# Performance work log

Measured on AMD Instinct MI355X. Metric: run time of the kernel, lower is better.

## Reference

```python
import jax, jax.numpy as jnp
import numpy as np

B, P, K, D, T = 512, 64, 8, 512, 50000


def setup_inputs() -> dict:
    key = jax.random.key(0)
    k1, k2, k3, k4, k5, k6 = jax.random.split(key, 6)
    return {
        "inputs": jax.random.normal(k1, (B, P, D), dtype=jnp.float32),
        "title_emb_mat": jax.random.normal(k2, (T, D), dtype=jnp.float32),
        "nbr_batch": jax.random.randint(k3, (B, P, K), 0, B, dtype=jnp.int32),
        "nbr_job": jax.random.randint(k4, (B, P, K), 0, P, dtype=jnp.int32),
        "nbr_title": jax.random.randint(k5, (B, P, K), 0, T, dtype=jnp.int32),
        "nbr_mask": jax.random.randint(k6, (B, P, K), 0, 2, dtype=jnp.int32),
    }


def reference(inputs, title_emb_mat, nbr_batch, nbr_job, nbr_title, nbr_mask):
    # inputs:        [B, P, D]  job embeddings per employee position
    # title_emb_mat: [T, Dt]    title embedding table (Dt == D here)
    # nbr_*:         [B, P, K]  padded metapath neighbor indices + validity mask
    mask = nbr_mask.astype(bool)                              # [B,P,K]
    ref_embs = inputs[nbr_batch, nbr_job]                     # [B,P,K,D] gather of neighbor job embs
    # attention logits: focal emb vs neighbor embs (raw inner product, exp-normalized)
    raw_s = jnp.einsum('bpd,bpkd->bpk', inputs, ref_embs)     # [B,P,K]
    logits = jnp.where(mask, raw_s, jnp.float32(-1e9))
    sim = jax.nn.softmax(logits, axis=-1) * mask              # exact zeros on padded slots;
    # an all-masked (i,pos) -> uniform softmax * 0 mask == 0 row (matches torch 'continue' -> zeros)
    ref_t_embs = title_emb_mat[nbr_title]                     # [B,P,K,Dt] gather of target-title embs
    graph_concat = jnp.einsum('bpk,bpkt->bpt', sim, ref_t_embs)  # [B,P,Dt]
    out = jnp.concatenate([inputs, graph_concat], axis=-1)    # [B,P,D+Dt]
    return out.reshape(B * P, D + title_emb_mat.shape[1])     # torch.cat over batch, axis=0
```

## Files before the change

kernel.cpp:

```cpp
#include <hip/hip_runtime.h>

#define BB 512
#define PP 64
#define KK 8
#define DD 512

typedef float v4f __attribute__((ext_vector_type(4)));


__device__ __forceinline__ void async_1k(const void* g, void* l) {
    __builtin_amdgcn_global_load_lds(
        (const __attribute__((address_space(1))) void*)g,
        (__attribute__((address_space(3))) void*)l,
        16, 0, 0);
}

__global__ __launch_bounds__(64) void han_meta_kernel(
    const float* __restrict__ inputs,
    const float* __restrict__ title,
    const int*   __restrict__ nbr_batch,
    const int*   __restrict__ nbr_job,
    const int*   __restrict__ nbr_title,
    const int*   __restrict__ nbr_mask,
    float*       __restrict__ out)
{
    __shared__ float lds_f[8192];

    const int lane = threadIdx.x;
    const int row  = __builtin_amdgcn_readfirstlane(blockIdx.x);

    const int* nb = nbr_batch + row * KK;
    const int* nj = nbr_job   + row * KK;
    const int* nt = nbr_title + row * KK;
    const int* nm = nbr_mask  + row * KK;
    int nbk[KK], njk[KK], ntk[KK], nmk[KK];
    #pragma unroll
    for (int k = 0; k < KK; ++k) {
        nbk[k] = __builtin_amdgcn_readfirstlane(nb[k]);
        njk[k] = __builtin_amdgcn_readfirstlane(nj[k]);
        ntk[k] = __builtin_amdgcn_readfirstlane(nt[k]);
        nmk[k] = __builtin_amdgcn_readfirstlane(nm[k]);
    }

    const unsigned focal_off = (unsigned)row * (DD * 4);
    unsigned goff[KK], toff[KK];
    #pragma unroll
    for (int k = 0; k < KK; ++k) {
        goff[k] = nmk[k] ? (unsigned)(nbk[k] * PP + njk[k]) * (DD * 4)
                         : focal_off;
        toff[k] = nmk[k] ? (unsigned)ntk[k] * (DD * 4)
                         : 0u;
    }

    const char* ibase = (const char*)inputs;
    const char* tbase = (const char*)title;
    char*       lbase = (char*)lds_f;
    const unsigned lo = (unsigned)lane * 16;

    #pragma unroll
    for (int k = 0; k < KK; ++k) {
        async_1k(ibase + goff[k] + lo,        lbase + k * 2048);
        async_1k(ibase + goff[k] + lo + 1024, lbase + k * 2048 + 1024);
    }

    const float4 fa = *(const float4*)(ibase + focal_off + lo);
    const float4 fb = *(const float4*)(ibase + focal_off + lo + 1024);

    #pragma unroll
    for (int k = 0; k < KK; ++k) {
        async_1k(tbase + toff[k] + lo,        lbase + 16384 + k * 2048);
        async_1k(tbase + toff[k] + lo + 1024, lbase + 16384 + k * 2048 + 1024);
    }

    asm volatile("s_waitcnt vmcnt(16)" ::: "memory");
    __builtin_amdgcn_sched_barrier(0);

    const float4* l4 = (const float4*)lds_f;
    float d[KK];
    #pragma unroll
    for (int k = 0; k < KK; ++k) {
        const float4 ga = l4[k * 128 + lane];
        const float4 gb = l4[k * 128 + 64 + lane];
        d[k] = fa.x*ga.x + fa.y*ga.y + fa.z*ga.z + fa.w*ga.w
             + fb.x*gb.x + fb.y*gb.y + fb.z*gb.z + fb.w*gb.w;
    }

    #pragma unroll
    for (int off = 32; off >= 1; off >>= 1) {
        #pragma unroll
        for (int k = 0; k < KK; ++k)
            d[k] += __shfl_xor(d[k], off, 64);
    }

    float logit[KK];
    #pragma unroll
    for (int k = 0; k < KK; ++k) logit[k] = nmk[k] ? d[k] : -1e9f;
    float m = logit[0];
    #pragma unroll
    for (int k = 1; k < KK; ++k) m = fmaxf(m, logit[k]);
    float e[KK];
    float s = 0.0f;
    #pragma unroll
    for (int k = 0; k < KK; ++k) {
        e[k] = expf(logit[k] - m);
        s += e[k];
    }
    const float inv = 1.0f / s;
    float w[KK];
    #pragma unroll
    for (int k = 0; k < KK; ++k) w[k] = nmk[k] ? e[k] * inv : 0.0f;

    asm volatile("s_waitcnt vmcnt(0)" ::: "memory");
    __builtin_amdgcn_sched_barrier(0);

    float4 oa = make_float4(0.f, 0.f, 0.f, 0.f);
    float4 ob = make_float4(0.f, 0.f, 0.f, 0.f);
    #pragma unroll
    for (int k = 0; k < KK; ++k) {
        const float4 ta = l4[1024 + k * 128 + lane];
        const float4 tb = l4[1024 + k * 128 + 64 + lane];
        oa.x += w[k]*ta.x; oa.y += w[k]*ta.y; oa.z += w[k]*ta.z; oa.w += w[k]*ta.w;
        ob.x += w[k]*tb.x; ob.y += w[k]*tb.y; ob.z += w[k]*tb.z; ob.w += w[k]*tb.w;
    }

    v4f* o4 = (v4f*)(out + (size_t)row * (2 * DD));
    v4f va = {fa.x, fa.y, fa.z, fa.w};
    v4f vb = {fb.x, fb.y, fb.z, fb.w};
    v4f vc = {oa.x, oa.y, oa.z, oa.w};
    v4f vd = {ob.x, ob.y, ob.z, ob.w};
    __builtin_nontemporal_store(va, o4 + lane);
    __builtin_nontemporal_store(vb, o4 + lane + 64);
    __builtin_nontemporal_store(vc, o4 + lane + 128);
    __builtin_nontemporal_store(vd, o4 + lane + 192);
}

extern "C" void kernel_launch(void* const* d_in, const int* in_sizes, int n_in,
                              void* d_out, int out_size, void* d_ws, size_t ws_size,
                              hipStream_t stream) {
    const float* inputs    = (const float*)d_in[0];
    const float* title     = (const float*)d_in[1];
    const int*   nbr_batch = (const int*)d_in[2];
    const int*   nbr_job   = (const int*)d_in[3];
    const int*   nbr_title = (const int*)d_in[4];
    const int*   nbr_mask  = (const int*)d_in[5];
    float*       out       = (float*)d_out;

    const int rows = BB * PP;
    dim3 grid(rows);
    dim3 block(64);

    han_meta_kernel<<<grid, block, 0, stream>>>(
        inputs, title, nbr_batch, nbr_job, nbr_title, nbr_mask, out);
}
```

Measured before the change: 318.6 us.

## Skip masked-slot gathers, reuse LDS for title rows, pack two rows per block

Masked neighbor slots no longer issue any global-to-LDS loads for either the job or title embeddings, which removes roughly half of the gather traffic with random masks. The title gather now goes into the same LDS region after the dot products finish, halving LDS per row so two rows (two waves) share a 128-thread block. The cost is that the title loads are serialized behind the neighbor dot products instead of being in flight at the same time, which lowers memory-level parallelism within a wave.

```diff
diff --git a/kernel.cpp b/kernel.cpp
--- a/kernel.cpp
+++ b/kernel.cpp
@@ -15,7 +15,7 @@
         16, 0, 0);
 }
 
-__global__ __launch_bounds__(64) void han_meta_kernel(
+__global__ __launch_bounds__(128) void han_meta_kernel(
     const float* __restrict__ inputs,
     const float* __restrict__ title,
     const int*   __restrict__ nbr_batch,
@@ -26,8 +26,11 @@
 {
     __shared__ float lds_f[8192];
 
-    const int lane = threadIdx.x;
-    const int row  = __builtin_amdgcn_readfirstlane(blockIdx.x);
+    const int lane = threadIdx.x & 63;
+    const int wrow = threadIdx.x >> 6;
+    const int row  = __builtin_amdgcn_readfirstlane(blockIdx.x * 2 + wrow);
+
+    char* lbase = (char*)(lds_f + wrow * 4096);
 
     const int* nb = nbr_batch + row * KK;
     const int* nj = nbr_job   + row * KK;
@@ -42,40 +45,27 @@
         nmk[k] = __builtin_amdgcn_readfirstlane(nm[k]);
     }
 
-    const unsigned focal_off = (unsigned)row * (DD * 4);
-    unsigned goff[KK], toff[KK];
-    #pragma unroll
-    for (int k = 0; k < KK; ++k) {
-        goff[k] = nmk[k] ? (unsigned)(nbk[k] * PP + njk[k]) * (DD * 4)
-                         : focal_off;
-        toff[k] = nmk[k] ? (unsigned)ntk[k] * (DD * 4)
-                         : 0u;
-    }
-
     const char* ibase = (const char*)inputs;
     const char* tbase = (const char*)title;
-    char*       lbase = (char*)lds_f;
+    const unsigned focal_off = (unsigned)row * (DD * 4);
     const unsigned lo = (unsigned)lane * 16;
 
     #pragma unroll
     for (int k = 0; k < KK; ++k) {
-        async_1k(ibase + goff[k] + lo,        lbase + k * 2048);
-        async_1k(ibase + goff[k] + lo + 1024, lbase + k * 2048 + 1024);
+        if (nmk[k]) {
+            const unsigned go = (unsigned)(nbk[k] * PP + njk[k]) * (DD * 4);
+            async_1k(ibase + go + lo,        lbase + k * 2048);
+            async_1k(ibase + go + lo + 1024, lbase + k * 2048 + 1024);
+        }
     }
 
     const float4 fa = *(const float4*)(ibase + focal_off + lo);
     const float4 fb = *(const float4*)(ibase + focal_off + lo + 1024);
 
-    #pragma unroll
-    for (int k = 0; k < KK; ++k) {
-        async_1k(tbase + toff[k] + lo,        lbase + 16384 + k * 2048);
-        async_1k(tbase + toff[k] + lo + 1024, lbase + 16384 + k * 2048 + 1024);
-    }
-
-    asm volatile("s_waitcnt vmcnt(16)" ::: "memory");
+    asm volatile("s_waitcnt vmcnt(0)" ::: "memory");
     __builtin_amdgcn_sched_barrier(0);
 
-    const float4* l4 = (const float4*)lds_f;
+    const float4* l4 = (const float4*)lbase;
     float d[KK];
     #pragma unroll
     for (int k = 0; k < KK; ++k) {
@@ -92,6 +82,18 @@
             d[k] += __shfl_xor(d[k], off, 64);
     }
 
+    asm volatile("s_waitcnt lgkmcnt(0)" ::: "memory");
+    __builtin_amdgcn_sched_barrier(0);
+
+    #pragma unroll
+    for (int k = 0; k < KK; ++k) {
+        if (nmk[k]) {
+            const unsigned to = (unsigned)ntk[k] * (DD * 4);
+            async_1k(tbase + to + lo,        lbase + k * 2048);
+            async_1k(tbase + to + lo + 1024, lbase + k * 2048 + 1024);
+        }
+    }
+
     float logit[KK];
     #pragma unroll
     for (int k = 0; k < KK; ++k) logit[k] = nmk[k] ? d[k] : -1e9f;
@@ -106,9 +108,6 @@
         s += e[k];
     }
     const float inv = 1.0f / s;
-    float w[KK];
-    #pragma unroll
-    for (int k = 0; k < KK; ++k) w[k] = nmk[k] ? e[k] * inv : 0.0f;
 
     asm volatile("s_waitcnt vmcnt(0)" ::: "memory");
     __builtin_amdgcn_sched_barrier(0);
@@ -117,10 +116,13 @@
     float4 ob = make_float4(0.f, 0.f, 0.f, 0.f);
     #pragma unroll
     for (int k = 0; k < KK; ++k) {
-        const float4 ta = l4[1024 + k * 128 + lane];
-        const float4 tb = l4[1024 + k * 128 + 64 + lane];
-        oa.x += w[k]*ta.x; oa.y += w[k]*ta.y; oa.z += w[k]*ta.z; oa.w += w[k]*ta.w;
-        ob.x += w[k]*tb.x; ob.y += w[k]*tb.y; ob.z += w[k]*tb.z; ob.w += w[k]*tb.w;
+        if (nmk[k]) {
+            const float w = e[k] * inv;
+            const float4 ta = l4[k * 128 + lane];
+            const float4 tb = l4[k * 128 + 64 + lane];
+            oa.x += w*ta.x; oa.y += w*ta.y; oa.z += w*ta.z; oa.w += w*ta.w;
+            ob.x += w*tb.x; ob.y += w*tb.y; ob.z += w*tb.z; ob.w += w*tb.w;
+        }
     }
 
     v4f* o4 = (v4f*)(out + (size_t)row * (2 * DD));
@@ -146,8 +148,8 @@
     float*       out       = (float*)d_out;
 
     const int rows = BB * PP;
-    dim3 grid(rows);
-    dim3 block(64);
+    dim3 grid(rows / 2);
+    dim3 block(128);
 
     han_meta_kernel<<<grid, block, 0, stream>>>(
         inputs, title, nbr_batch, nbr_job, nbr_title, nbr_mask, out);
```

New measurement: 297.6 us. 1.07x faster.
